# Performance work log

Hardware: AMD Instinct MI355X
Metric: run time of the kernel (lower is better)

## Reference

```python
import jax, jax.numpy as jnp
import numpy as np

TOKENS = 4096
IN_FEATURES = 4096
OUT_FEATURES = 4096
NNZ = 512  # nonzeros per output row, multiple of 4 so vectorize-pad is a no-op


def setup_inputs() -> dict:
    key = jax.random.key(0)
    k1, k2, k3, k4 = jax.random.split(key, 4)
    x = jax.random.normal(k1, (TOKENS, IN_FEATURES), dtype=jnp.float32)
    w = jax.random.normal(k2, (OUT_FEATURES, NNZ), dtype=jnp.float32)
    # sorted per-row column indices, mimicking nonzero() order of a pruned row
    mask = jnp.sort(
        jax.random.randint(k3, (OUT_FEATURES, NNZ), 0, IN_FEATURES, dtype=jnp.int32),
        axis=-1,
    )
    b = jax.random.normal(k4, (OUT_FEATURES,), dtype=jnp.float32)
    return {"input": x, "condensed_weight": w, "input_mask": mask, "bias": b}


def reference(input, condensed_weight, input_mask, bias):
    # y[t, o] = sum_k input[t, input_mask[o, k]] * condensed_weight[o, k] + bias[o]
    # Scatter condensed rows back to a dense [O, In] weight, then GEMM.
    # .add handles duplicate / padded (index 0, weight 0) entries exactly like
    # the gather-multiply-reduce formulation.
    O, K = condensed_weight.shape
    In = input.shape[-1]
    rows = jnp.arange(O, dtype=input_mask.dtype)[:, None]  # [O, 1]
    W = jnp.zeros((O, In), dtype=condensed_weight.dtype).at[rows, input_mask].add(condensed_weight)
    return input @ W.T + bias
```

## Files before the change

### kernel.cpp

```cpp
#include <hip/hip_runtime.h>
#include <hip/hip_bf16.h>
#include <stdint.h>

#define TOKENS 4096
#define IN_F   4096
#define OUT_F  4096
#define NNZ    512

using floatx4 = __attribute__((ext_vector_type(4))) float;
using bf16x8  = __attribute__((ext_vector_type(8))) __bf16;

__device__ __forceinline__ unsigned short f2bf(float f) {
    unsigned int u = __float_as_uint(f);
    u += 0x7FFFu + ((u >> 16) & 1u);
    return (unsigned short)(u >> 16);
}

__global__ __launch_bounds__(256) void prep_fused(
        const float* __restrict__ x,
        const float* __restrict__ w,
        const int*   __restrict__ mask,
        unsigned short* __restrict__ Xb,
        unsigned short* __restrict__ Wb) {
    __shared__ unsigned short rows[4][IN_F];
    const int b = blockIdx.x;
    const int t = threadIdx.x;

    if (b < 1024) {
        const int wave = t >> 6;
        const int lane = t & 63;
        const int rrow = b * 4 + wave;
        unsigned short* row = rows[wave];
        uint4* rv = (uint4*)row;
        const uint4 z = make_uint4(0u, 0u, 0u, 0u);
#pragma unroll
        for (int j = 0; j < 8; ++j) rv[lane + 64 * j] = z;

        const int base = rrow * NNZ;
        const int4*   m4 = (const int4*)(mask + base);
        const float4* w4 = (const float4*)(w + base);
        const int4   ma = m4[2 * lane], mb2 = m4[2 * lane + 1];
        const float4 wa = w4[2 * lane], wb2 = w4[2 * lane + 1];
        const int   mk[8] = {ma.x, ma.y, ma.z, ma.w, mb2.x, mb2.y, mb2.z, mb2.w};
        const float wk[8] = {wa.x, wa.y, wa.z, wa.w, wb2.x, wb2.y, wb2.z, wb2.w};

        int   cur = (lane == 0) ? -1 : mask[base + 8 * lane - 1];
        float s   = 0.0f;
        bool  own = false;
#pragma unroll
        for (int e = 0; e < 8; ++e) {
            if (mk[e] != cur) {
                if (own) row[cur] = f2bf(s);
                cur = mk[e]; s = wk[e]; own = true;
            } else if (own) {
                s += wk[e];
            }
        }
        if (own) {
            int g = 8 * lane + 8;
            while (g < NNZ && mask[base + g] == cur) { s += w[base + g]; ++g; }
            row[cur] = f2bf(s);
        }

        uint4* out = (uint4*)(Wb + (size_t)rrow * IN_F);
#pragma unroll
        for (int j = 0; j < 8; ++j) out[lane + 64 * j] = rv[lane + 64 * j];
    } else {
        const int b1 = b - 1024;
        const float4* xv = (const float4*)x;
        uint4* xo = (uint4*)Xb;
#pragma unroll
        for (int it = 0; it < 4; ++it) {
            const int i = b1 * 256 + t + it * 524288;
            float4 a = xv[2 * i];
            float4 c = xv[2 * i + 1];
            uint4 o;
            o.x = (unsigned)f2bf(a.x) | ((unsigned)f2bf(a.y) << 16);
            o.y = (unsigned)f2bf(a.z) | ((unsigned)f2bf(a.w) << 16);
            o.z = (unsigned)f2bf(c.x) | ((unsigned)f2bf(c.y) << 16);
            o.w = (unsigned)f2bf(c.z) | ((unsigned)f2bf(c.w) << 16);
            xo[i] = o;
        }
    }
}


#define GLL16(src, dst) \
    __builtin_amdgcn_global_load_lds((__attribute__((address_space(1))) void*)(src), \
                                     (__attribute__((address_space(3))) void*)(dst), 16, 0, 0)

__global__ __launch_bounds__(512, 2) void gemm_bt_bias(
        const unsigned short* __restrict__ A,
        const unsigned short* __restrict__ B,
        const float* __restrict__ bias,
        float* __restrict__ C) {
    __shared__ unsigned short As[2][16384];
    __shared__ unsigned short Bs[2][16384];

    const int tid  = threadIdx.x;
    const int wave = tid >> 6;
    const int lane = tid & 63;
    const int lq   = lane >> 4;
    const int lm   = lane & 15;
    const int lm7  = lm & 7;
    const int wm2  = wave >> 2;
    const int wn4  = wave & 3;

    const int bid = blockIdx.x;
    const int swz = (bid & 7) * 32 + (bid >> 3);
    const int m0  = (swz >> 4) << 8;
    const int n0  = (swz & 15) << 8;

    const int r   = tid >> 3;
    const int cse = ((tid & 7) ^ (r & 7)) * 8;
    const int oAX0 = (m0 + r)       * IN_F + cse;
    const int oAX1 = (m0 + 128 + r) * IN_F + cse;
    const int oAY0 = (m0 +  64 + r) * IN_F + cse;
    const int oAY1 = (m0 + 192 + r) * IN_F + cse;
    const int bc_  = (r >> 5) * 64 + (r & 31);
    const int oBU0 = (n0 + bc_)        * IN_F + cse;
    const int oBU1 = (n0 + 128 + bc_)  * IN_F + cse;
    const int oBV0 = (n0 +  32 + bc_)  * IN_F + cse;
    const int oBV1 = (n0 + 160 + bc_)  * IN_F + cse;
    const int wofs = wave * 512;

#define STAGE_AX(bb, kk) { GLL16(A + oAX0 + (kk), &As[bb][        wofs]); \
                           GLL16(A + oAX1 + (kk), &As[bb][ 4096 + wofs]); }
#define STAGE_AY(bb, kk) { GLL16(A + oAY0 + (kk), &As[bb][ 8192 + wofs]); \
                           GLL16(A + oAY1 + (kk), &As[bb][12288 + wofs]); }
#define STAGE_BU(bb, kk) { GLL16(B + oBU0 + (kk), &Bs[bb][        wofs]); \
                           GLL16(B + oBU1 + (kk), &Bs[bb][ 4096 + wofs]); }
#define STAGE_BV(bb, kk) { GLL16(B + oBV0 + (kk), &Bs[bb][ 8192 + wofs]); \
                           GLL16(B + oBV1 + (kk), &Bs[bb][12288 + wofs]); }

    const int ck0 = (lq ^ lm7) * 8;
    const int ck1 = ck0 ^ 32;
    const int aX  = (wm2 * 64 + lm) * 64;
    const int aY  = aX + 8192;
    const int bU  = (wn4 * 32 + lm) * 64;
    const int bV  = bU + 8192;

    floatx4 acc[8][4] = {};
    bf16x8 af[4][2], bu[2][2], bv[2][2];

    STAGE_AX(0, 0); STAGE_BU(0, 0); STAGE_BV(0, 0); STAGE_AY(0, 0);
    STAGE_AX(1, 64); STAGE_BU(1, 64); STAGE_BV(1, 64);
    asm volatile("s_waitcnt vmcnt(6)" ::: "memory");
    __builtin_amdgcn_s_barrier();

#define TILE_STEP(T, BB)                                                          \
    {                                                                             \
        const unsigned short* sA = As[BB];                                        \
        const unsigned short* sB = Bs[BB];                                        \
        const int kk1 = ((T) + 1 < 64 ? (T) + 1 : 63) * 64;                       \
        const int kk2 = ((T) + 2 < 64 ? (T) + 2 : 63) * 64;                       \
                                                      \
        _Pragma("unroll")                                                         \
        for (int mi = 0; mi < 4; ++mi) {                                          \
            af[mi][0] = *(const bf16x8*)(sA + aX + mi * 1024 + ck0);              \
            af[mi][1] = *(const bf16x8*)(sA + aX + mi * 1024 + ck1);              \
        }                                                                         \
        _Pragma("unroll")                                                         \
        for (int ni = 0; ni < 2; ++ni) {                                          \
            bu[ni][0] = *(const bf16x8*)(sB + bU + ni * 1024 + ck0);              \
            bu[ni][1] = *(const bf16x8*)(sB + bU + ni * 1024 + ck1);              \
        }                                                                         \
        STAGE_AY((BB) ^ 1, kk1);                                                  \
        asm volatile("s_waitcnt lgkmcnt(8)" ::: "memory");                        \
        __builtin_amdgcn_s_barrier();                                             \
        asm volatile("s_waitcnt lgkmcnt(0)" ::: "memory");                        \
        __builtin_amdgcn_s_setprio(1);                                            \
        _Pragma("unroll")                                                         \
        for (int mi = 0; mi < 4; ++mi)                                            \
            _Pragma("unroll")                                                     \
            for (int ni = 0; ni < 2; ++ni) {                                      \
                acc[mi][ni] = __builtin_amdgcn_mfma_f32_16x16x32_bf16(            \
                    af[mi][0], bu[ni][0], acc[mi][ni], 0, 0, 0);                  \
                acc[mi][ni] = __builtin_amdgcn_mfma_f32_16x16x32_bf16(            \
                    af[mi][1], bu[ni][1], acc[mi][ni], 0, 0, 0);                  \
            }                                                                     \
        __builtin_amdgcn_s_setprio(0);                                            \
        __builtin_amdgcn_s_barrier();                                             \
                                                      \
        _Pragma("unroll")                                                         \
        for (int ni = 0; ni < 2; ++ni) {                                          \
            bv[ni][0] = *(const bf16x8*)(sB + bV + ni * 1024 + ck0);              \
            bv[ni][1] = *(const bf16x8*)(sB + bV + ni * 1024 + ck1);              \
        }                                                                         \
        STAGE_AX((BB), kk2);                                                      \
        __builtin_amdgcn_s_barrier();                                             \
        asm volatile("s_waitcnt lgkmcnt(0)" ::: "memory");                        \
        __builtin_amdgcn_s_setprio(1);                                            \
        _Pragma("unroll")                                                         \
        for (int mi = 0; mi < 4; ++mi)                                            \
            _Pragma("unroll")                                                     \
            for (int ni = 0; ni < 2; ++ni) {                                      \
                acc[mi][2 + ni] = __builtin_amdgcn_mfma_f32_16x16x32_bf16(        \
                    af[mi][0], bv[ni][0], acc[mi][2 + ni], 0, 0, 0);              \
                acc[mi][2 + ni] = __builtin_amdgcn_mfma_f32_16x16x32_bf16(        \
                    af[mi][1], bv[ni][1], acc[mi][2 + ni], 0, 0, 0);              \
            }                                                                     \
        __builtin_amdgcn_s_setprio(0);                                            \
        __builtin_amdgcn_s_barrier();                                             \
                                                      \
        _Pragma("unroll")                                                         \
        for (int mi = 0; mi < 4; ++mi) {                                          \
            af[mi][0] = *(const bf16x8*)(sA + aY + mi * 1024 + ck0);              \
            af[mi][1] = *(const bf16x8*)(sA + aY + mi * 1024 + ck1);              \
        }                                                                         \
        STAGE_BU((BB), kk2);                                                      \
        __builtin_amdgcn_s_barrier();                                             \
        asm volatile("s_waitcnt lgkmcnt(0)" ::: "memory");                        \
        __builtin_amdgcn_s_setprio(1);                                            \
        _Pragma("unroll")                                                         \
        for (int mi = 0; mi < 4; ++mi)                                            \
            _Pragma("unroll")                                                     \
            for (int ni = 0; ni < 2; ++ni) {                                      \
                acc[4 + mi][2 + ni] = __builtin_amdgcn_mfma_f32_16x16x32_bf16(    \
                    af[mi][0], bv[ni][0], acc[4 + mi][2 + ni], 0, 0, 0);          \
                acc[4 + mi][2 + ni] = __builtin_amdgcn_mfma_f32_16x16x32_bf16(    \
                    af[mi][1], bv[ni][1], acc[4 + mi][2 + ni], 0, 0, 0);          \
            }                                                                     \
        __builtin_amdgcn_s_setprio(0);                                            \
        __builtin_amdgcn_s_barrier();                                             \
                                \
        STAGE_BV((BB), kk2);                                                      \
        __builtin_amdgcn_s_barrier();                                             \
        __builtin_amdgcn_s_setprio(1);                                            \
        _Pragma("unroll")                                                         \
        for (int mi = 0; mi < 4; ++mi)                                            \
            _Pragma("unroll")                                                     \
            for (int ni = 0; ni < 2; ++ni) {                                      \
                acc[4 + mi][ni] = __builtin_amdgcn_mfma_f32_16x16x32_bf16(        \
                    af[mi][0], bu[ni][0], acc[4 + mi][ni], 0, 0, 0);              \
                acc[4 + mi][ni] = __builtin_amdgcn_mfma_f32_16x16x32_bf16(        \
                    af[mi][1], bu[ni][1], acc[4 + mi][ni], 0, 0, 0);              \
            }                                                                     \
        __builtin_amdgcn_s_setprio(0);                                            \
        asm volatile("s_waitcnt vmcnt(6)" ::: "memory");                          \
        __builtin_amdgcn_s_barrier();                                             \
    }

    for (int tt = 0; tt < 32; ++tt) {
        TILE_STEP(2 * tt,     0);
        TILE_STEP(2 * tt + 1, 1);
    }

#pragma unroll
    for (int ni = 0; ni < 4; ++ni) {
        const int n = n0 + wn4 * 64 + ni * 16 + lm;
        const float bb = bias[n];
#pragma unroll
        for (int mi = 0; mi < 8; ++mi) {
            const int mb = m0 + wm2 * 128 + mi * 16 + lq * 4;
#pragma unroll
            for (int rr = 0; rr < 4; ++rr) {
                __builtin_nontemporal_store(acc[mi][ni][rr] + bb,
                                            &C[(size_t)(mb + rr) * OUT_F + n]);
            }
        }
    }
}

extern "C" void kernel_launch(void* const* d_in, const int* in_sizes, int n_in,
                              void* d_out, int out_size, void* d_ws, size_t ws_size,
                              hipStream_t stream) {
    const float* x    = (const float*)d_in[0];
    const float* w    = (const float*)d_in[1];
    const int*   mask = (const int*)d_in[2];
    const float* bias = (const float*)d_in[3];
    float* out = (float*)d_out;

    unsigned short* Xb = (unsigned short*)d_ws;
    unsigned short* Wb = Xb + (size_t)TOKENS * IN_F;

    prep_fused<<<3072, 256, 0, stream>>>(x, w, mask, Xb, Wb);
    gemm_bt_bias<<<dim3(256), dim3(512), 0, stream>>>(Xb, Wb, bias, out);
}
```

Before: 254.8 us.

## Switch GEMM inner loop from 16x16x32 to 32x32x16 bf16 MFMA tiles

```diff
diff --git a/kernel.cpp b/kernel.cpp
--- a/kernel.cpp
+++ b/kernel.cpp
@@ -7,8 +7,8 @@
 #define OUT_F  4096
 #define NNZ    512
 
-using floatx4 = __attribute__((ext_vector_type(4))) float;
-using bf16x8  = __attribute__((ext_vector_type(8))) __bf16;
+using floatx16 = __attribute__((ext_vector_type(16))) float;
+using bf16x8   = __attribute__((ext_vector_type(8))) __bf16;
 
 __device__ __forceinline__ unsigned short f2bf(float f) {
     unsigned int u = __float_as_uint(f);
@@ -100,9 +100,9 @@
     const int tid  = threadIdx.x;
     const int wave = tid >> 6;
     const int lane = tid & 63;
-    const int lq   = lane >> 4;
-    const int lm   = lane & 15;
-    const int lm7  = lm & 7;
+    const int rl   = lane & 31;
+    const int hi   = lane >> 5;
+    const int r7   = rl & 7;
     const int wm2  = wave >> 2;
     const int wn4  = wave & 3;
 
@@ -133,15 +133,13 @@
 #define STAGE_BV(bb, kk) { GLL16(B + oBV0 + (kk), &Bs[bb][ 8192 + wofs]); \
                            GLL16(B + oBV1 + (kk), &Bs[bb][12288 + wofs]); }
 
-    const int ck0 = (lq ^ lm7) * 8;
-    const int ck1 = ck0 ^ 32;
-    const int aX  = (wm2 * 64 + lm) * 64;
-    const int aY  = aX + 8192;
-    const int bU  = (wn4 * 32 + lm) * 64;
-    const int bV  = bU + 8192;
-
-    floatx4 acc[8][4] = {};
-    bf16x8 af[4][2], bu[2][2], bv[2][2];
+    const int aX = (wm2 * 64 + rl) * 64;
+    const int aY = aX + 8192;
+    const int bU = (wn4 * 32 + rl) * 64;
+    const int bV = bU + 8192;
+
+    floatx16 acc[4][2] = {};
+    bf16x8 af[2][4], bu[4], bv[4];
 
     STAGE_AX(0, 0); STAGE_BU(0, 0); STAGE_BV(0, 0); STAGE_AY(0, 0);
     STAGE_AX(1, 64); STAGE_BU(1, 64); STAGE_BV(1, 64);
@@ -154,88 +152,74 @@
         const unsigned short* sB = Bs[BB];                                        \
         const int kk1 = ((T) + 1 < 64 ? (T) + 1 : 63) * 64;                       \
         const int kk2 = ((T) + 2 < 64 ? (T) + 2 : 63) * 64;                       \
-                                                      \
-        _Pragma("unroll")                                                         \
-        for (int mi = 0; mi < 4; ++mi) {                                          \
-            af[mi][0] = *(const bf16x8*)(sA + aX + mi * 1024 + ck0);              \
-            af[mi][1] = *(const bf16x8*)(sA + aX + mi * 1024 + ck1);              \
-        }                                                                         \
-        _Pragma("unroll")                                                         \
-        for (int ni = 0; ni < 2; ++ni) {                                          \
-            bu[ni][0] = *(const bf16x8*)(sB + bU + ni * 1024 + ck0);              \
-            bu[ni][1] = *(const bf16x8*)(sB + bU + ni * 1024 + ck1);              \
-        }                                                                         \
+                                          \
+        _Pragma("unroll")                                                         \
+        for (int mi = 0; mi < 2; ++mi)                                            \
+            _Pragma("unroll")                                                     \
+            for (int ks = 0; ks < 4; ++ks)                                        \
+                af[mi][ks] = *(const bf16x8*)(sA + aX + mi * 2048 +               \
+                                              (((ks * 2 + hi) ^ r7) * 8));        \
+        _Pragma("unroll")                                                         \
+        for (int ks = 0; ks < 4; ++ks)                                            \
+            bu[ks] = *(const bf16x8*)(sB + bU + (((ks * 2 + hi) ^ r7) * 8));      \
         STAGE_AY((BB) ^ 1, kk1);                                                  \
         asm volatile("s_waitcnt lgkmcnt(8)" ::: "memory");                        \
         __builtin_amdgcn_s_barrier();                                             \
         asm volatile("s_waitcnt lgkmcnt(0)" ::: "memory");                        \
         __builtin_amdgcn_s_setprio(1);                                            \
         _Pragma("unroll")                                                         \
-        for (int mi = 0; mi < 4; ++mi)                                            \
-            _Pragma("unroll")                                                     \
-            for (int ni = 0; ni < 2; ++ni) {                                      \
-                acc[mi][ni] = __builtin_amdgcn_mfma_f32_16x16x32_bf16(            \
-                    af[mi][0], bu[ni][0], acc[mi][ni], 0, 0, 0);                  \
-                acc[mi][ni] = __builtin_amdgcn_mfma_f32_16x16x32_bf16(            \
-                    af[mi][1], bu[ni][1], acc[mi][ni], 0, 0, 0);                  \
-            }                                                                     \
-        __builtin_amdgcn_s_setprio(0);                                            \
-        __builtin_amdgcn_s_barrier();                                             \
-                                                      \
-        _Pragma("unroll")                                                         \
-        for (int ni = 0; ni < 2; ++ni) {                                          \
-            bv[ni][0] = *(const bf16x8*)(sB + bV + ni * 1024 + ck0);              \
-            bv[ni][1] = *(const bf16x8*)(sB + bV + ni * 1024 + ck1);              \
-        }                                                                         \
+        for (int ks = 0; ks < 4; ++ks)                                            \
+            _Pragma("unroll")                                                     \
+            for (int mi = 0; mi < 2; ++mi)                                        \
+                acc[mi][0] = __builtin_amdgcn_mfma_f32_32x32x16_bf16(             \
+                    af[mi][ks], bu[ks], acc[mi][0], 0, 0, 0);                     \
+        __builtin_amdgcn_s_setprio(0);                                            \
+        __builtin_amdgcn_s_barrier();                                             \
+                                          \
+        _Pragma("unroll")                                                         \
+        for (int ks = 0; ks < 4; ++ks)                                            \
+            bv[ks] = *(const bf16x8*)(sB + bV + (((ks * 2 + hi) ^ r7) * 8));      \
         STAGE_AX((BB), kk2);                                                      \
         __builtin_amdgcn_s_barrier();                                             \
         asm volatile("s_waitcnt lgkmcnt(0)" ::: "memory");                        \
         __builtin_amdgcn_s_setprio(1);                                            \
         _Pragma("unroll")                                                         \
-        for (int mi = 0; mi < 4; ++mi)                                            \
-            _Pragma("unroll")                                                     \
-            for (int ni = 0; ni < 2; ++ni) {                                      \
-                acc[mi][2 + ni] = __builtin_amdgcn_mfma_f32_16x16x32_bf16(        \
-                    af[mi][0], bv[ni][0], acc[mi][2 + ni], 0, 0, 0);              \
-                acc[mi][2 + ni] = __builtin_amdgcn_mfma_f32_16x16x32_bf16(        \
-                    af[mi][1], bv[ni][1], acc[mi][2 + ni], 0, 0, 0);              \
-            }                                                                     \
-        __builtin_amdgcn_s_setprio(0);                                            \
-        __builtin_amdgcn_s_barrier();                                             \
-                                                      \
-        _Pragma("unroll")                                                         \
-        for (int mi = 0; mi < 4; ++mi) {                                          \
-            af[mi][0] = *(const bf16x8*)(sA + aY + mi * 1024 + ck0);              \
-            af[mi][1] = *(const bf16x8*)(sA + aY + mi * 1024 + ck1);              \
-        }                                                                         \
+        for (int ks = 0; ks < 4; ++ks)                                            \
+            _Pragma("unroll")                                                     \
+            for (int mi = 0; mi < 2; ++mi)                                        \
+                acc[mi][1] = __builtin_amdgcn_mfma_f32_32x32x16_bf16(             \
+                    af[mi][ks], bv[ks], acc[mi][1], 0, 0, 0);                     \
+        __builtin_amdgcn_s_setprio(0);                                            \
+        __builtin_amdgcn_s_barrier();                                             \
+                                          \
+        _Pragma("unroll")                                                         \
+        for (int mi = 0; mi < 2; ++mi)                                            \
+            _Pragma("unroll")                                                     \
+            for (int ks = 0; ks < 4; ++ks)                                        \
+                af[mi][ks] = *(const bf16x8*)(sA + aY + mi * 2048 +               \
+                                              (((ks * 2 + hi) ^ r7) * 8));        \
         STAGE_BU((BB), kk2);                                                      \
         __builtin_amdgcn_s_barrier();                                             \
         asm volatile("s_waitcnt lgkmcnt(0)" ::: "memory");                        \
         __builtin_amdgcn_s_setprio(1);                                            \
         _Pragma("unroll")                                                         \
-        for (int mi = 0; mi < 4; ++mi)                                            \
-            _Pragma("unroll")                                                     \
-            for (int ni = 0; ni < 2; ++ni) {                                      \
-                acc[4 + mi][2 + ni] = __builtin_amdgcn_mfma_f32_16x16x32_bf16(    \
-                    af[mi][0], bv[ni][0], acc[4 + mi][2 + ni], 0, 0, 0);          \
-                acc[4 + mi][2 + ni] = __builtin_amdgcn_mfma_f32_16x16x32_bf16(    \
-                    af[mi][1], bv[ni][1], acc[4 + mi][2 + ni], 0, 0, 0);          \
-            }                                                                     \
-        __builtin_amdgcn_s_setprio(0);                                            \
-        __builtin_amdgcn_s_barrier();                                             \
-                                \
+        for (int ks = 0; ks < 4; ++ks)                                            \
+            _Pragma("unroll")                                                     \
+            for (int mi = 0; mi < 2; ++mi)                                        \
+                acc[2 + mi][1] = __builtin_amdgcn_mfma_f32_32x32x16_bf16(         \
+                    af[mi][ks], bv[ks], acc[2 + mi][1], 0, 0, 0);                 \
+        __builtin_amdgcn_s_setprio(0);                                            \
+        __builtin_amdgcn_s_barrier();                                             \
+                     \
         STAGE_BV((BB), kk2);                                                      \
         __builtin_amdgcn_s_barrier();                                             \
         __builtin_amdgcn_s_setprio(1);                                            \
         _Pragma("unroll")                                                         \
-        for (int mi = 0; mi < 4; ++mi)                                            \
-            _Pragma("unroll")                                                     \
-            for (int ni = 0; ni < 2; ++ni) {                                      \
-                acc[4 + mi][ni] = __builtin_amdgcn_mfma_f32_16x16x32_bf16(        \
-                    af[mi][0], bu[ni][0], acc[4 + mi][ni], 0, 0, 0);              \
-                acc[4 + mi][ni] = __builtin_amdgcn_mfma_f32_16x16x32_bf16(        \
-                    af[mi][1], bu[ni][1], acc[4 + mi][ni], 0, 0, 0);              \
-            }                                                                     \
+        for (int ks = 0; ks < 4; ++ks)                                            \
+            _Pragma("unroll")                                                     \
+            for (int mi = 0; mi < 2; ++mi)                                        \
+                acc[2 + mi][0] = __builtin_amdgcn_mfma_f32_32x32x16_bf16(         \
+                    af[mi][ks], bu[ks], acc[2 + mi][0], 0, 0, 0);                 \
         __builtin_amdgcn_s_setprio(0);                                            \
         asm volatile("s_waitcnt vmcnt(6)" ::: "memory");                          \
         __builtin_amdgcn_s_barrier();                                             \
@@ -247,16 +231,16 @@
     }
 
 #pragma unroll
-    for (int ni = 0; ni < 4; ++ni) {
-        const int n = n0 + wn4 * 64 + ni * 16 + lm;
+    for (int ni = 0; ni < 2; ++ni) {
+        const int n = n0 + wn4 * 64 + ni * 32 + rl;
         const float bb = bias[n];
 #pragma unroll
-        for (int mi = 0; mi < 8; ++mi) {
-            const int mb = m0 + wm2 * 128 + mi * 16 + lq * 4;
-#pragma unroll
-            for (int rr = 0; rr < 4; ++rr) {
-                __builtin_nontemporal_store(acc[mi][ni][rr] + bb,
-                                            &C[(size_t)(mb + rr) * OUT_F + n]);
+        for (int mi = 0; mi < 4; ++mi) {
+            const int mbase = m0 + wm2 * 128 + mi * 32 + hi * 4;
+#pragma unroll
+            for (int rr = 0; rr < 16; ++rr) {
+                const int m = mbase + (rr & 3) + 8 * (rr >> 2);
+                C[(size_t)m * OUT_F + n] = acc[mi][ni][rr] + bb;
             }
         }
     }
```

New measurement: 260.5 us. 2.3% more time.
